# Optimization experiments

Measured on AMD Instinct MI355X. Metric: run time of the kernel, lower is better.

The kernel has to match this reference:

```python
import jax, jax.numpy as jnp
import numpy as np
from functools import partial

VOCAB, D, H, L, T_MAX = 32000, 1024, 16, 8, 1024
HD = D // H
HIDDEN = int(D * 2.67)  # 2734, matches int(n_embd*hidden_mult)


def setup_inputs() -> dict:
    key = jax.random.key(0)
    ks = jax.random.split(key, 9)
    s = 0.02
    return {
        "idx": jax.random.randint(ks[0], (2, 1024), 0, VOCAB),
        "W_emb": jax.random.normal(ks[1], (VOCAB, D), jnp.float32) * s,  # tied with lm_head
        "norm1_w": jnp.ones((L, D), jnp.float32),
        "Wqkv": jax.random.normal(ks[2], (L, D, 3 * D), jnp.float32) * s,
        "Wout": jax.random.normal(ks[3], (L, D, D), jnp.float32) * s,
        "norm2_w": jnp.ones((L, D), jnp.float32),
        "Wg": jax.random.normal(ks[4], (L, D, HIDDEN), jnp.float32) * s,
        "Wu": jax.random.normal(ks[5], (L, D, HIDDEN), jnp.float32) * s,
        "Wd": jax.random.normal(ks[6], (L, HIDDEN, D), jnp.float32) * s,
        "final_norm_w": jnp.ones((D,), jnp.float32),
    }


def _rmsnorm(x, w, eps=1e-6):
    rms = jnp.sqrt(jnp.mean(x * x, axis=-1, keepdims=True) + eps)
    return x / rms * w


def _rope(x, cos_f, sin_f):
    # x: [B,H,T,hd]; cos_f/sin_f: [T, hd//2]
    x1, x2 = x[..., : HD // 2], x[..., HD // 2 :]
    c = cos_f[None, None]
    s = sin_f[None, None]
    return jnp.concatenate([x1 * c - x2 * s, x1 * s + x2 * c], axis=-1)


def _forward(idx, W_emb, norm1_w, Wqkv, Wout, norm2_w, Wg, Wu, Wd, final_norm_w):
    B, T = idx.shape
    # RoPE tables (buffers in the torch module)
    inv_freq = 1.0 / (10000.0 ** (jnp.arange(0, HD, 2, dtype=jnp.float32) / HD))
    ang = jnp.arange(T, dtype=jnp.float32)[:, None] * inv_freq[None, :]  # [T, hd//2]
    cos_f, sin_f = jnp.cos(ang), jnp.sin(ang)
    causal = jnp.tril(jnp.ones((T, T), dtype=bool))  # [T,T]
    scale = 1.0 / jnp.sqrt(jnp.float32(HD))

    def block(x, params):
        n1, wqkv, wout, n2, wg, wu, wd = params
        h = _rmsnorm(x, n1)
        qkv = (h @ wqkv).reshape(B, T, 3, H, HD).transpose(2, 0, 3, 1, 4)  # [3,B,H,T,hd]
        q, k, v = qkv[0], qkv[1], qkv[2]
        q = _rope(q, cos_f, sin_f)
        k = _rope(k, cos_f, sin_f)
        attn = jnp.einsum("bhqd,bhkd->bhqk", q, k) * scale
        attn = jnp.where(causal[None, None], attn, -jnp.inf)
        attn = jax.nn.softmax(attn, axis=-1)
        o = jnp.einsum("bhqk,bhkd->bhqd", attn, v)
        o = o.transpose(0, 2, 1, 3).reshape(B, T, D) @ wout
        x = x + o
        h2 = _rmsnorm(x, n2)
        x = x + (jax.nn.silu(h2 @ wg) * (h2 @ wu)) @ wd
        return x, None

    x = W_emb[idx]  # [B,T,D]
    x, _ = jax.lax.scan(block, x, (norm1_w, Wqkv, Wout, norm2_w, Wg, Wu, Wd))
    x = _rmsnorm(x, final_norm_w)
    return x @ W_emb.T  # tied lm_head -> [B,T,VOCAB]


def reference(idx, W_emb, norm1_w, Wqkv, Wout, norm2_w, Wg, Wu, Wd, final_norm_w):
    return _forward(idx, W_emb, norm1_w, Wqkv, Wout, norm2_w, Wg, Wu, Wd, final_norm_w)
```

## Files before the change

### kernel.cpp

```cpp
#include <hip/hip_runtime.h>
#include <cstdint>
#include <cmath>

#define D_MODEL 1024
#define T_SEQ   1024
#define NHEAD   16
#define NLAYER  8
#define HID     2734
#define HID_PAD 2816
#define NTOK    2048
#define VOCAB   32000

typedef __bf16 bf16x8 __attribute__((ext_vector_type(8)));
typedef __bf16 bf16x4 __attribute__((ext_vector_type(4)));
typedef float  f32x4  __attribute__((ext_vector_type(4)));

__device__ inline bf16x4 to_bf4(float a, float b, float c, float d) {
  bf16x4 t; t[0] = (__bf16)a; t[1] = (__bf16)b; t[2] = (__bf16)c; t[3] = (__bf16)d; return t;
}

__device__ inline void gload16(const __bf16* g, __bf16* l) {
  __builtin_amdgcn_global_load_lds(
      (const __attribute__((address_space(1))) void*)g,
      (__attribute__((address_space(3))) void*)l, 16, 0, 0);
}

__global__ __launch_bounds__(256) void embed_kernel(const int* __restrict__ idx,
                                                    const float* __restrict__ W,
                                                    float* __restrict__ x) {
  int t = blockIdx.x;
  int v = idx[t];
  float4 val = *(const float4*)&W[(size_t)v * D_MODEL + threadIdx.x * 4];
  *(float4*)&x[(size_t)t * D_MODEL + threadIdx.x * 4] = val;
}

__global__ __launch_bounds__(256) void rmsnorm_kernel(const float* __restrict__ x,
                                                      const float* __restrict__ w,
                                                      __bf16* __restrict__ out) {
  int row = blockIdx.x;
  int tid = threadIdx.x;
  float4 v = *(const float4*)&x[(size_t)row * D_MODEL + tid * 4];
  float s = v.x * v.x + v.y * v.y + v.z * v.z + v.w * v.w;
#pragma unroll
  for (int m = 32; m >= 1; m >>= 1) s += __shfl_xor(s, m, 64);
  __shared__ float red[4];
  if ((tid & 63) == 0) red[tid >> 6] = s;
  __syncthreads();
  float tot = red[0] + red[1] + red[2] + red[3];
  float inv = rsqrtf(tot * (1.0f / (float)D_MODEL) + 1e-6f);
  float4 wv = *(const float4*)&w[tid * 4];
  bf16x4 o4 = to_bf4(v.x * inv * wv.x, v.y * inv * wv.y, v.z * inv * wv.z, v.w * inv * wv.w);
  *(bf16x4*)&out[(size_t)row * D_MODEL + tid * 4] = o4;
}

__global__ __launch_bounds__(256) void rope_table_kernel(float* __restrict__ tab) {
  int p = blockIdx.x * 256 + threadIdx.x;
  int t = p >> 5, i = p & 31;
  float freq = exp2f(-(float)i * (13.287712379549449f / 32.0f));
  float sn, cs;
  sincosf((float)t * freq, &sn, &cs);
  tab[p] = cs;
  tab[32768 + p] = sn;
}

__global__ __launch_bounds__(256) void tp5_kernel(
    const float* __restrict__ Wqkv, const float* __restrict__ Wout,
    const float* __restrict__ Wg, const float* __restrict__ Wu,
    const float* __restrict__ Wd,
    __bf16* __restrict__ wqkvT, __bf16* __restrict__ woutT,
    __bf16* __restrict__ wguT, __bf16* __restrict__ wdT) {
  __shared__ __bf16 tile[64][65];
  int t = blockIdx.x;
  const float* in;
  __bf16* out;
  int R, C, Ro, rmul, roff, tr;
  if (t < 768)        { in = Wqkv; out = wqkvT; R = 1024; C = 3072; Ro = 1024; rmul = 1; roff = 0; tr = 16; }
  else if (t < 1024)  { t -= 768;  in = Wout; out = woutT; R = 1024; C = 1024; Ro = 1024; rmul = 1; roff = 0; tr = 16; }
  else if (t < 1728)  { t -= 1024; in = Wg; out = wguT; R = 1024; C = HID; Ro = 1024; rmul = 2; roff = 0; tr = 16; }
  else if (t < 2432)  { t -= 1728; in = Wu; out = wguT; R = 1024; C = HID; Ro = 1024; rmul = 2; roff = 1; tr = 16; }
  else                { t -= 2432; in = Wd; out = wdT; R = HID; C = 1024; Ro = HID_PAD; rmul = 1; roff = 0; tr = 44; }
  int r0 = (t % tr) * 64, c0 = (t / tr) * 64;
  int tid = threadIdx.x;
  bool fullc = (c0 + 64 <= C);
#pragma unroll
  for (int i = 0; i < 4; ++i) {
    int ri = i * 16 + (tid >> 4);
    int ci = (tid & 15) * 4;
    int r = r0 + ri;
    float4 v = {0.f, 0.f, 0.f, 0.f};
    if (r < R) {
      const float* p = in + (size_t)r * C + c0 + ci;
      if (fullc) {
        v = *(const float4*)p;
      } else {
        int c = c0 + ci;
        if (c + 0 < C) v.x = p[0];
        if (c + 1 < C) v.y = p[1];
        if (c + 2 < C) v.z = p[2];
        if (c + 3 < C) v.w = p[3];
      }
    }
    tile[ri][ci + 0] = (__bf16)v.x;
    tile[ri][ci + 1] = (__bf16)v.y;
    tile[ri][ci + 2] = (__bf16)v.z;
    tile[ri][ci + 3] = (__bf16)v.w;
  }
  __syncthreads();
#pragma unroll
  for (int i = 0; i < 4; ++i) {
    int oc = i * 16 + (tid >> 4);
    int orr = (tid & 15) * 4;
    bf16x4 tv;
    tv[0] = tile[orr + 0][oc];
    tv[1] = tile[orr + 1][oc];
    tv[2] = tile[orr + 2][oc];
    tv[3] = tile[orr + 3][oc];
    *(bf16x4*)&out[((size_t)(c0 + oc) * rmul + roff) * Ro + r0 + orr] = tv;
  }
}

__global__ __launch_bounds__(256) void convert_bf16_kernel(const float* __restrict__ in,
                                                           __bf16* __restrict__ out, int n4) {
  for (int i = blockIdx.x * 256 + threadIdx.x; i < n4; i += gridDim.x * 256) {
    float4 v = ((const float4*)in)[i];
    ((bf16x4*)out)[i] = to_bf4(v.x, v.y, v.z, v.w);
  }
}

template <int BM, int BN, int WM, int WN, int EPI>
__global__ __launch_bounds__(WM * WN * 64, 2) void gemm8(
    const __bf16* __restrict__ A, const __bf16* __restrict__ B,
    const float* __restrict__ Cin, void* __restrict__ Cout,
    int K, int ldc) {
  constexpr int NTH = WM * WN * 64;
  constexpr int MF = BM / (16 * WM);
  constexpr int MG = (MF + 3) / 4;
  constexpr int CL = (MF < 4) ? MF : 4;
  constexpr int LA = (BM * 4) / NTH;
  constexpr int LB = (BN * 4) / NTH;
  static_assert(BN / WN == 64, "NF must be 4");
  __shared__ __align__(16) __bf16 lds[(BM + BN) * 128];

  const int tid = threadIdx.x;
  const int lane = tid & 63, wid = tid >> 6;
  const int wr = wid / WN, wn = wid % WN;
  const int lr = lane & 15, lg = lane >> 4;

  const int gx = gridDim.x;
  const int nwg = gx * gridDim.y;
  const int orig = blockIdx.y * gx + blockIdx.x;
  const int q = nwg >> 3, r8 = nwg & 7;
  const int xcd = orig & 7, loc = orig >> 3;
  const int swz = ((xcd < r8) ? xcd * (q + 1) : r8 * (q + 1) + (xcd - r8) * q) + loc;
  const int brow = (swz % gx) * BM;
  const int bcol = (swz / gx) * BN;

  const __bf16* pAg[LA];
  const __bf16* pBg[LB];
  int opA[LA], opB[LB];
#pragma unroll
  for (int i = 0; i < LA; ++i) {
    int p = tid + i * NTH;
    int row = ((p >> 6) << 4) | (p & 15), j = (p >> 4) & 3;
    pAg[i] = A + (size_t)(brow + row) * K + j * 8;
    opA[i] = p * 8;
  }
#pragma unroll
  for (int i = 0; i < LB; ++i) {
    int p = tid + i * NTH;
    int row = ((p >> 6) << 4) | (p & 15), j = (p >> 4) & 3;
    pBg[i] = B + (size_t)(bcol + row) * K + j * 8;
    opB[i] = p * 8;
  }

  const int ntiles = K >> 6;

  auto STAGE_A = [&](int v, int kkq) {
    int vs = v < ntiles ? v : ntiles - 1;
    int ko = vs * 64 + kkq * 32;
    int sa = (v & 1) * (BM * 64) + kkq * (BM * 32);
#pragma unroll
    for (int i = 0; i < LA; ++i) gload16(pAg[i] + ko, lds + sa + opA[i]);
  };
  auto STAGE_B = [&](int v, int kkq) {
    int vs = v < ntiles ? v : ntiles - 1;
    int ko = vs * 64 + kkq * 32;
    int sb = BM * 128 + (v & 1) * (BN * 64) + kkq * (BN * 32);
#pragma unroll
    for (int i = 0; i < LB; ++i) gload16(pBg[i] + ko, lds + sb + opB[i]);
  };

  f32x4 acc[MF][4];
#pragma unroll
  for (int m = 0; m < MF; ++m)
#pragma unroll
    for (int n = 0; n < 4; ++n) acc[m][n] = (f32x4){0.f, 0.f, 0.f, 0.f};

  STAGE_A(0, 0); STAGE_B(0, 0);
  STAGE_A(0, 1); STAGE_B(0, 1);
  STAGE_A(1, 0); STAGE_B(1, 0);

  const int fragoff = lg * 128 + lr * 8;

  if constexpr (MF == 8) {
    for (int u = 0; u < ntiles; ++u) {
      const int buf = u & 1;
#pragma unroll
      for (int kk = 0; kk < 2; ++kk) {
        const int v = (kk == 0) ? u + 1 : u + 2;
        const int kkq = kk ^ 1;
        const __bf16* Ab = lds + buf * (BM * 64) + kk * (BM * 32);
        const __bf16* Bb = lds + BM * 128 + buf * (BN * 64) + kk * (BN * 32);
        asm volatile("s_waitcnt vmcnt(8)" ::: "memory");
        __builtin_amdgcn_sched_barrier(0);
        __builtin_amdgcn_s_barrier();
        __builtin_amdgcn_sched_barrier(0);
        STAGE_A(v, kkq);
        bf16x8 bfr[4], af0[4];
#pragma unroll
        for (int n = 0; n < 4; ++n)
          bfr[n] = *(const bf16x8*)(Bb + (wn * 64 + n * 16) * 32 + fragoff);
#pragma unroll
        for (int i = 0; i < 4; ++i)
          af0[i] = *(const bf16x8*)(Ab + (wr * 128 + i * 16) * 32 + fragoff);
        asm volatile("s_waitcnt lgkmcnt(0)" ::: "memory");
        __builtin_amdgcn_sched_barrier(0);
        __builtin_amdgcn_s_setprio(1);
#pragma unroll
        for (int i = 0; i < 4; ++i)
#pragma unroll
          for (int n = 0; n < 4; ++n)
            acc[i][n] = __builtin_amdgcn_mfma_f32_16x16x32_bf16(af0[i], bfr[n], acc[i][n], 0, 0, 0);
        __builtin_amdgcn_s_setprio(0);
        __builtin_amdgcn_s_barrier();
        STAGE_B(v, kkq);
        bf16x8 af1[4];
#pragma unroll
        for (int i = 0; i < 4; ++i)
          af1[i] = *(const bf16x8*)(Ab + (wr * 128 + 64 + i * 16) * 32 + fragoff);
        asm volatile("s_waitcnt lgkmcnt(0)" ::: "memory");
        __builtin_amdgcn_sched_barrier(0);
        __builtin_amdgcn_s_setprio(1);
#pragma unroll
        for (int i = 0; i < 4; ++i)
#pragma unroll
          for (int n = 0; n < 4; ++n)
            acc[4 + i][n] = __builtin_amdgcn_mfma_f32_16x16x32_bf16(af1[i], bfr[n], acc[4 + i][n], 0, 0, 0);
        __builtin_amdgcn_s_setprio(0);
        __builtin_amdgcn_s_barrier();
      }
    }
  } else {
    for (int u = 0; u < ntiles; ++u) {
      const int buf = u & 1;
#pragma unroll
      for (int kk = 0; kk < 2; ++kk) {
        if constexpr (LA + LB == 3) asm volatile("s_waitcnt vmcnt(6)" ::: "memory");
        else                        asm volatile("s_waitcnt vmcnt(8)" ::: "memory");
        __builtin_amdgcn_sched_barrier(0);
        __builtin_amdgcn_s_barrier();
        __builtin_amdgcn_sched_barrier(0);
        const int v = (kk == 0) ? u + 1 : u + 2;
        const int kkq = kk ^ 1;
        STAGE_A(v, kkq);
        STAGE_B(v, kkq);
        const __bf16* Ab = lds + buf * (BM * 64) + kk * (BM * 32);
        const __bf16* Bb = lds + BM * 128 + buf * (BN * 64) + kk * (BN * 32);
        bf16x8 bfr[4];
#pragma unroll
        for (int n = 0; n < 4; ++n)
          bfr[n] = *(const bf16x8*)(Bb + (wn * 64 + n * 16) * 32 + fragoff);
#pragma unroll
        for (int mg = 0; mg < MG; ++mg) {
          bf16x8 afr[CL];
#pragma unroll
          for (int i = 0; i < CL; ++i)
            afr[i] = *(const bf16x8*)(Ab + (wr * (BM / WM) + (mg * 4 + i) * 16) * 32 + fragoff);
          __builtin_amdgcn_s_setprio(1);
#pragma unroll
          for (int i = 0; i < CL; ++i)
#pragma unroll
            for (int n = 0; n < 4; ++n)
              acc[mg * 4 + i][n] =
                  __builtin_amdgcn_mfma_f32_16x16x32_bf16(afr[i], bfr[n], acc[mg * 4 + i][n], 0, 0, 0);
          __builtin_amdgcn_s_setprio(0);
        }
      }
    }
  }

#pragma unroll
  for (int m = 0; m < MF; ++m) {
#pragma unroll
    for (int n = 0; n < 4; ++n) {
#pragma unroll
      for (int rr = 0; rr < 4; ++rr) {
        int row = brow + wr * (BM / WM) + m * 16 + lg * 4 + rr;
        int col = bcol + wn * 64 + n * 16 + lr;
        size_t off = (size_t)row * ldc + col;
        float vv = acc[m][n][rr];
        if (EPI == 0) {
          ((float*)Cout)[off] = vv;
        } else if (EPI == 1) {
          ((float*)Cout)[off] = Cin[off] + vv;
        } else if (EPI == 2) {
          float gv = Cin[off];
          ((__bf16*)Cout)[off] = (__bf16)(gv / (1.f + __expf(-gv)) * vv);
        } else if (EPI == 3) {
          ((__bf16*)Cout)[off] = (__bf16)vv;
        } else {
          float uv = __shfl_xor(vv, 1);
          if ((lr & 1) == 0) {
            float r = vv / (1.f + __expf(-vv)) * uv;
            ((__bf16*)Cout)[(size_t)row * ldc + (col >> 1)] = (__bf16)r;
          }
        }
      }
    }
  }
}

__device__ inline void rope_chunk(const __bf16* p, const float* __restrict__ tab,
                                  int t, int d0, bf16x8& olo, bf16x8& ohi) {
  bf16x8 a8 = *(const bf16x8*)p;
  bf16x8 b8 = *(const bf16x8*)(p + 32);
  const float* ct = tab + t * 32 + d0;
  const float* st = tab + 32768 + t * 32 + d0;
  float4 c0 = *(const float4*)ct, c1 = *(const float4*)(ct + 4);
  float4 s0 = *(const float4*)st, s1 = *(const float4*)(st + 4);
  float cs[8] = {c0.x, c0.y, c0.z, c0.w, c1.x, c1.y, c1.z, c1.w};
  float ss[8] = {s0.x, s0.y, s0.z, s0.w, s1.x, s1.y, s1.z, s1.w};
#pragma unroll
  for (int j = 0; j < 8; ++j) {
    float av = (float)a8[j], bv = (float)b8[j];
    olo[j] = (__bf16)(av * cs[j] - bv * ss[j]);
    ohi[j] = (__bf16)(av * ss[j] + bv * cs[j]);
  }
}

__global__ __launch_bounds__(256) void prep_kernel(const __bf16* __restrict__ qkv,
                                                   const float* __restrict__ tab,
                                                   __bf16* __restrict__ Qr,
                                                   __bf16* __restrict__ Kr,
                                                   __bf16* __restrict__ Vt) {
  __shared__ __bf16 lsV[64][72];
  const int tid = threadIdx.x;
  const int bh = blockIdx.y, b = bh >> 4, h = bh & 15;
  const int t0 = blockIdx.x * 64;
  const size_t qbase = (size_t)b * T_SEQ * 3072 + h * 64;

  int row = tid >> 2, pc = tid & 3;
  int t = t0 + row;
  int tl = t & 1023;
  {
    int d0 = pc * 8;
    bf16x8 olo, ohi;
    rope_chunk(qkv + qbase + (size_t)t * 3072 + d0, tab, tl, d0, olo, ohi);
    __bf16* qo = Qr + ((size_t)bh * T_SEQ + t) * 64;
    *(bf16x8*)(qo + d0) = olo;
    *(bf16x8*)(qo + d0 + 32) = ohi;
    rope_chunk(qkv + qbase + (size_t)t * 3072 + 1024 + d0, tab, tl, d0, olo, ohi);
    __bf16* ko = Kr + ((size_t)bh * T_SEQ + t) * 64;
    *(bf16x8*)(ko + d0) = olo;
    *(bf16x8*)(ko + d0 + 32) = ohi;
  }
  {
    int c = pc * 16;
    bf16x8 v0 = *(const bf16x8*)(qkv + qbase + (size_t)t * 3072 + 2048 + c);
    bf16x8 v1 = *(const bf16x8*)(qkv + qbase + (size_t)t * 3072 + 2048 + c + 8);
    *(bf16x8*)&lsV[row][c] = v0;
    *(bf16x8*)&lsV[row][c + 8] = v1;
  }
  __syncthreads();
  {
    int d = tid >> 2, tc = (tid & 3) * 16;
    bf16x8 o0, o1;
#pragma unroll
    for (int j = 0; j < 8; ++j) o0[j] = lsV[tc + j][d];
#pragma unroll
    for (int j = 0; j < 8; ++j) o1[j] = lsV[tc + 8 + j][d];
    __bf16* vo = Vt + ((size_t)bh * 64 + d) * T_SEQ + t0 + tc;
    *(bf16x8*)vo = o0;
    *(bf16x8*)(vo + 8) = o1;
  }
}

__global__ __launch_bounds__(256) void attn_kernel(const __bf16* __restrict__ Qr,
                                                   const __bf16* __restrict__ Kr,
                                                   const __bf16* __restrict__ Vt,
                                                   __bf16* __restrict__ o) {
  __shared__ __align__(16) __bf16 lds[28672];
  const int tid = threadIdx.x;
  const int lane = tid & 63, w = tid >> 6;
  const int lr = lane & 15, lg = lane >> 4;
  const int bh = blockIdx.y, b = bh >> 4, h = bh & 15;
  const int qb = blockIdx.x, q0 = qb * 64;
  const __bf16* Qg = Qr + ((size_t)bh * T_SEQ + q0) * 64;
  const __bf16* Kg = Kr + (size_t)bh * T_SEQ * 64;
  const __bf16* Vg = Vt + (size_t)bh * 64 * T_SEQ;
  const float scale = 0.125f;

  {
    int row = ((tid >> 6) << 4) | (tid & 15);
    int j = (tid >> 4) & 3;
    gload16(Qg + row * 64 + j * 8, lds + tid * 8);
    gload16(Qg + row * 64 + 32 + j * 8, lds + 2048 + tid * 8);
  }

  f32x4 accO[4];
#pragma unroll
  for (int n = 0; n < 4; ++n) accO[n] = (f32x4){0.f, 0.f, 0.f, 0.f};
  float mrow[4], lrow[4];
#pragma unroll
  for (int r = 0; r < 4; ++r) { mrow[r] = -1e30f; lrow[r] = 0.f; }

  const int ntile = ((q0 + 63) >> 7) + 1;
  __bf16* Pw = lds + 20480 + w * 2048;

  for (int tt = 0; tt < ntile; ++tt) {
    const int j0 = tt * 128;
    __syncthreads();
#pragma unroll
    for (int i = 0; i < 2; ++i) {
      int p = tid + i * 256;
      int row = ((p >> 6) << 4) | (p & 15), j = (p >> 4) & 3;
      const __bf16* src = Kg + (size_t)(j0 + row) * 64 + j * 8;
      gload16(src, lds + 4096 + p * 8);
      gload16(src + 32, lds + 8192 + p * 8);
    }
#pragma unroll
    for (int s = 0; s < 4; ++s) {
      int d = ((tid >> 6) << 4) | (tid & 15), j = (tid >> 4) & 3;
      gload16(Vg + (size_t)d * T_SEQ + j0 + s * 32 + j * 8, lds + 12288 + s * 2048 + tid * 8);
    }
    __syncthreads();

    f32x4 s4[8];
#pragma unroll
    for (int n = 0; n < 8; ++n) s4[n] = (f32x4){0.f, 0.f, 0.f, 0.f};
#pragma unroll
    for (int kk = 0; kk < 2; ++kk) {
      bf16x8 aq = *(const bf16x8*)(lds + kk * 2048 + (w * 64 + lg * 16 + lr) * 8);
      __builtin_amdgcn_s_setprio(1);
#pragma unroll
      for (int jf = 0; jf < 8; ++jf) {
        bf16x8 bk = *(const bf16x8*)(lds + 4096 + kk * 4096 + (jf * 64 + lg * 16 + lr) * 8);
        s4[jf] = __builtin_amdgcn_mfma_f32_16x16x32_bf16(aq, bk, s4[jf], 0, 0, 0);
      }
      __builtin_amdgcn_s_setprio(0);
    }

    float pm[4];
#pragma unroll
    for (int r = 0; r < 4; ++r) pm[r] = -1e30f;
#pragma unroll
    for (int jf = 0; jf < 8; ++jf) {
      int gj = j0 + jf * 16 + lr;
#pragma unroll
      for (int r = 0; r < 4; ++r) {
        int gq = q0 + w * 16 + lg * 4 + r;
        float sv = s4[jf][r] * scale;
        if (gj > gq) sv = -1e30f;
        s4[jf][r] = sv;
        pm[r] = fmaxf(pm[r], sv);
      }
    }
#pragma unroll
    for (int r = 0; r < 4; ++r) {
#pragma unroll
      for (int m = 8; m >= 1; m >>= 1) pm[r] = fmaxf(pm[r], __shfl_xor(pm[r], m, 64));
    }
    float alpha[4];
#pragma unroll
    for (int r = 0; r < 4; ++r) {
      float mn = fmaxf(mrow[r], pm[r]);
      alpha[r] = expf(mrow[r] - mn);
      mrow[r] = mn;
    }
    float ps[4] = {0.f, 0.f, 0.f, 0.f};
#pragma unroll
    for (int jf = 0; jf < 8; ++jf) {
#pragma unroll
      for (int r = 0; r < 4; ++r) {
        float p = expf(s4[jf][r] - mrow[r]);
        s4[jf][r] = p;
        ps[r] += p;
      }
    }
#pragma unroll
    for (int r = 0; r < 4; ++r) {
#pragma unroll
      for (int m = 8; m >= 1; m >>= 1) ps[r] += __shfl_xor(ps[r], m, 64);
      lrow[r] = lrow[r] * alpha[r] + ps[r];
    }
#pragma unroll
    for (int n = 0; n < 4; ++n) {
#pragma unroll
      for (int r = 0; r < 4; ++r) accO[n][r] *= alpha[r];
    }

#pragma unroll
    for (int jf = 0; jf < 8; ++jf) {
      int s = jf >> 1;
      int rem = ((jf & 1) << 4) + lr;
      int base = s * 512 + (rem >> 3) * 128 + (rem & 7);
#pragma unroll
      for (int r = 0; r < 4; ++r) {
        int qloc = lg * 4 + r;
        Pw[base + qloc * 8] = (__bf16)s4[jf][r];
      }
    }
    asm volatile("s_waitcnt lgkmcnt(0)" ::: "memory");
    __builtin_amdgcn_sched_barrier(0);

#pragma unroll
    for (int s = 0; s < 4; ++s) {
      bf16x8 pa = *(const bf16x8*)(Pw + s * 512 + (lg * 16 + lr) * 8);
      __builtin_amdgcn_s_setprio(1);
#pragma unroll
      for (int nd = 0; nd < 4; ++nd) {
        bf16x8 bv = *(const bf16x8*)(lds + 12288 + s * 2048 + (nd * 64 + lg * 16 + lr) * 8);
        accO[nd] = __builtin_amdgcn_mfma_f32_16x16x32_bf16(pa, bv, accO[nd], 0, 0, 0);
      }
      __builtin_amdgcn_s_setprio(0);
    }
  }

#pragma unroll
  for (int nd = 0; nd < 4; ++nd) {
#pragma unroll
    for (int r = 0; r < 4; ++r) {
      int gq = q0 + w * 16 + lg * 4 + r;
      float val = accO[nd][r] / lrow[r];
      o[(size_t)(b * T_SEQ + gq) * D_MODEL + h * 64 + nd * 16 + lr] = (__bf16)val;
    }
  }
}

extern "C" void kernel_launch(void* const* d_in, const int* in_sizes, int n_in,
                              void* d_out, int out_size, void* d_ws, size_t ws_size,
                              hipStream_t stream) {
  const int*   idx     = (const int*)d_in[0];
  const float* W_emb   = (const float*)d_in[1];
  const float* norm1_w = (const float*)d_in[2];
  const float* Wqkv    = (const float*)d_in[3];
  const float* Wout    = (const float*)d_in[4];
  const float* norm2_w = (const float*)d_in[5];
  const float* Wg      = (const float*)d_in[6];
  const float* Wu      = (const float*)d_in[7];
  const float* Wd      = (const float*)d_in[8];
  const float* fnorm   = (const float*)d_in[9];
  float* out = (float*)d_out;

  float*  x    = (float*)d_ws;
  float*  tab  = x + (size_t)NTOK * D_MODEL;
  __bf16* qkvb = (__bf16*)(tab + 2 * 32768);
  __bf16* hb   = qkvb + (size_t)NTOK * 3 * D_MODEL;
  __bf16* ob   = hb + (size_t)NTOK * D_MODEL;
  __bf16* ga   = ob + (size_t)NTOK * D_MODEL;
  __bf16* Qrb  = ga + (size_t)NTOK * HID_PAD;
  __bf16* Krb  = Qrb + (size_t)32 * T_SEQ * 64;
  __bf16* Vtb  = Krb + (size_t)32 * T_SEQ * 64;
  __bf16* wbuf = Vtb + (size_t)32 * T_SEQ * 64;

  __bf16* wqkvT = wbuf;
  __bf16* woutT = wqkvT + (size_t)3 * D_MODEL * D_MODEL;
  __bf16* wguT  = woutT + (size_t)D_MODEL * D_MODEL;
  __bf16* wdT   = wguT + (size_t)2 * HID_PAD * D_MODEL;

  embed_kernel<<<NTOK, 256, 0, stream>>>(idx, W_emb, x);
  rope_table_kernel<<<128, 256, 0, stream>>>(tab);

  for (int l = 0; l < NLAYER; ++l) {
    tp5_kernel<<<3136, 256, 0, stream>>>(
        Wqkv + (size_t)l * D_MODEL * 3 * D_MODEL,
        Wout + (size_t)l * D_MODEL * D_MODEL,
        Wg + (size_t)l * D_MODEL * HID,
        Wu + (size_t)l * D_MODEL * HID,
        Wd + (size_t)l * HID * D_MODEL,
        wqkvT, woutT, wguT, wdT);

    rmsnorm_kernel<<<NTOK, 256, 0, stream>>>(x, norm1_w + (size_t)l * D_MODEL, hb);
    gemm8<128, 256, 2, 4, 3><<<dim3(16, 12), 512, 0, stream>>>(
        hb, wqkvT, nullptr, qkvb, D_MODEL, 3 * D_MODEL);
    prep_kernel<<<dim3(16, 32), 256, 0, stream>>>(qkvb, tab, Qrb, Krb, Vtb);
    attn_kernel<<<dim3(16, 32), 256, 0, stream>>>(Qrb, Krb, Vtb, ob);
    gemm8<128, 64, 4, 1, 1><<<dim3(16, 16), 256, 0, stream>>>(
        ob, woutT, x, x, D_MODEL, D_MODEL);
    rmsnorm_kernel<<<NTOK, 256, 0, stream>>>(x, norm2_w + (size_t)l * D_MODEL, hb);
    gemm8<256, 256, 2, 4, 4><<<dim3(8, 22), 512, 0, stream>>>(
        hb, wguT, nullptr, ga, D_MODEL, HID_PAD);
    gemm8<128, 64, 4, 1, 1><<<dim3(16, 16), 256, 0, stream>>>(
        ga, wdT, x, x, HID_PAD, D_MODEL);
  }

  rmsnorm_kernel<<<NTOK, 256, 0, stream>>>(x, fnorm, hb);
  convert_bf16_kernel<<<2048, 256, 0, stream>>>(W_emb, wbuf, VOCAB * D_MODEL / 4);
  gemm8<256, 256, 2, 4, 0><<<dim3(8, 125), 512, 0, stream>>>(
      hb, wbuf, nullptr, out, D_MODEL, VOCAB);
}
```

Before: 1.780 ms.

## Fuse RoPE and V transpose into QKV GEMM epilogue; pair causal attention blocks

The QKV GEMM gets a new epilogue that applies rotary embedding to Q and K and writes the transposed V directly into the attention layouts. This removes the separate prep kernel and the intermediate bf16 QKV buffer. Separately, the attention kernel now processes two complementary query blocks per workgroup (qp and 15-qp) to balance causal work, which halves the grid. The trade-offs are narrower, less coalesced epilogue stores and fewer attention workgroups.

```diff
diff --git a/kernel.cpp b/kernel.cpp
--- a/kernel.cpp
+++ b/kernel.cpp
@@ -131,7 +131,9 @@
 __global__ __launch_bounds__(WM * WN * 64, 2) void gemm8(
     const __bf16* __restrict__ A, const __bf16* __restrict__ B,
     const float* __restrict__ Cin, void* __restrict__ Cout,
-    int K, int ldc) {
+    int K, int ldc,
+    const float* __restrict__ Tab, __bf16* __restrict__ Qr,
+    __bf16* __restrict__ Kr, __bf16* __restrict__ Vt) {
   constexpr int NTH = WM * WN * 64;
   constexpr int MF = BM / (16 * WM);
   constexpr int MG = (MF + 3) / 4;
@@ -289,99 +291,66 @@
     }
   }
 
-#pragma unroll
-  for (int m = 0; m < MF; ++m) {
-#pragma unroll
-    for (int n = 0; n < 4; ++n) {
-#pragma unroll
-      for (int rr = 0; rr < 4; ++rr) {
-        int row = brow + wr * (BM / WM) + m * 16 + lg * 4 + rr;
-        int col = bcol + wn * 64 + n * 16 + lr;
-        size_t off = (size_t)row * ldc + col;
-        float vv = acc[m][n][rr];
-        if (EPI == 0) {
-          ((float*)Cout)[off] = vv;
-        } else if (EPI == 1) {
-          ((float*)Cout)[off] = Cin[off] + vv;
-        } else if (EPI == 2) {
-          float gv = Cin[off];
-          ((__bf16*)Cout)[off] = (__bf16)(gv / (1.f + __expf(-gv)) * vv);
-        } else if (EPI == 3) {
-          ((__bf16*)Cout)[off] = (__bf16)vv;
-        } else {
-          float uv = __shfl_xor(vv, 1);
-          if ((lr & 1) == 0) {
-            float r = vv / (1.f + __expf(-vv)) * uv;
-            ((__bf16*)Cout)[(size_t)row * ldc + (col >> 1)] = (__bf16)r;
+  if constexpr (EPI == 5) {
+    const int colw = bcol + wn * 64;
+    const int secw = colw >> 10;
+    const int h = (colw >> 6) & 15;
+#pragma unroll
+    for (int m = 0; m < MF; ++m) {
+      int row0 = brow + wr * (BM / WM) + m * 16 + lg * 4;
+      int bb = row0 >> 10;
+      int t0 = row0 & 1023;
+      int bh = bb * 16 + h;
+      if (secw < 2) {
+        __bf16* base = (secw == 0 ? Qr : Kr) + ((size_t)bh * T_SEQ + t0) * 64;
+#pragma unroll
+        for (int n = 0; n < 2; ++n) {
+          int din = n * 16 + lr;
+#pragma unroll
+          for (int rr = 0; rr < 4; ++rr) {
+            float a = acc[m][n][rr], b2 = acc[m][n + 2][rr];
+            float cs = Tab[(t0 + rr) * 32 + din];
+            float sn = Tab[32768 + (t0 + rr) * 32 + din];
+            base[(size_t)rr * 64 + din]      = (__bf16)(a * cs - b2 * sn);
+            base[(size_t)rr * 64 + din + 32] = (__bf16)(a * sn + b2 * cs);
           }
         }
-      }
-    }
-  }
-}
-
-__device__ inline void rope_chunk(const __bf16* p, const float* __restrict__ tab,
-                                  int t, int d0, bf16x8& olo, bf16x8& ohi) {
-  bf16x8 a8 = *(const bf16x8*)p;
-  bf16x8 b8 = *(const bf16x8*)(p + 32);
-  const float* ct = tab + t * 32 + d0;
-  const float* st = tab + 32768 + t * 32 + d0;
-  float4 c0 = *(const float4*)ct, c1 = *(const float4*)(ct + 4);
-  float4 s0 = *(const float4*)st, s1 = *(const float4*)(st + 4);
-  float cs[8] = {c0.x, c0.y, c0.z, c0.w, c1.x, c1.y, c1.z, c1.w};
-  float ss[8] = {s0.x, s0.y, s0.z, s0.w, s1.x, s1.y, s1.z, s1.w};
-#pragma unroll
-  for (int j = 0; j < 8; ++j) {
-    float av = (float)a8[j], bv = (float)b8[j];
-    olo[j] = (__bf16)(av * cs[j] - bv * ss[j]);
-    ohi[j] = (__bf16)(av * ss[j] + bv * cs[j]);
-  }
-}
-
-__global__ __launch_bounds__(256) void prep_kernel(const __bf16* __restrict__ qkv,
-                                                   const float* __restrict__ tab,
-                                                   __bf16* __restrict__ Qr,
-                                                   __bf16* __restrict__ Kr,
-                                                   __bf16* __restrict__ Vt) {
-  __shared__ __bf16 lsV[64][72];
-  const int tid = threadIdx.x;
-  const int bh = blockIdx.y, b = bh >> 4, h = bh & 15;
-  const int t0 = blockIdx.x * 64;
-  const size_t qbase = (size_t)b * T_SEQ * 3072 + h * 64;
-
-  int row = tid >> 2, pc = tid & 3;
-  int t = t0 + row;
-  int tl = t & 1023;
-  {
-    int d0 = pc * 8;
-    bf16x8 olo, ohi;
-    rope_chunk(qkv + qbase + (size_t)t * 3072 + d0, tab, tl, d0, olo, ohi);
-    __bf16* qo = Qr + ((size_t)bh * T_SEQ + t) * 64;
-    *(bf16x8*)(qo + d0) = olo;
-    *(bf16x8*)(qo + d0 + 32) = ohi;
-    rope_chunk(qkv + qbase + (size_t)t * 3072 + 1024 + d0, tab, tl, d0, olo, ohi);
-    __bf16* ko = Kr + ((size_t)bh * T_SEQ + t) * 64;
-    *(bf16x8*)(ko + d0) = olo;
-    *(bf16x8*)(ko + d0 + 32) = ohi;
-  }
-  {
-    int c = pc * 16;
-    bf16x8 v0 = *(const bf16x8*)(qkv + qbase + (size_t)t * 3072 + 2048 + c);
-    bf16x8 v1 = *(const bf16x8*)(qkv + qbase + (size_t)t * 3072 + 2048 + c + 8);
-    *(bf16x8*)&lsV[row][c] = v0;
-    *(bf16x8*)&lsV[row][c + 8] = v1;
-  }
-  __syncthreads();
-  {
-    int d = tid >> 2, tc = (tid & 3) * 16;
-    bf16x8 o0, o1;
-#pragma unroll
-    for (int j = 0; j < 8; ++j) o0[j] = lsV[tc + j][d];
-#pragma unroll
-    for (int j = 0; j < 8; ++j) o1[j] = lsV[tc + 8 + j][d];
-    __bf16* vo = Vt + ((size_t)bh * 64 + d) * T_SEQ + t0 + tc;
-    *(bf16x8*)vo = o0;
-    *(bf16x8*)(vo + 8) = o1;
+      } else {
+#pragma unroll
+        for (int n = 0; n < 4; ++n) {
+          int din = n * 16 + lr;
+          bf16x4 pk;
+#pragma unroll
+          for (int rr = 0; rr < 4; ++rr) pk[rr] = (__bf16)acc[m][n][rr];
+          *(bf16x4*)&Vt[((size_t)bh * 64 + din) * T_SEQ + t0] = pk;
+        }
+      }
+    }
+  } else {
+#pragma unroll
+    for (int m = 0; m < MF; ++m) {
+#pragma unroll
+      for (int n = 0; n < 4; ++n) {
+#pragma unroll
+        for (int rr = 0; rr < 4; ++rr) {
+          int row = brow + wr * (BM / WM) + m * 16 + lg * 4 + rr;
+          int col = bcol + wn * 64 + n * 16 + lr;
+          size_t off = (size_t)row * ldc + col;
+          float vv = acc[m][n][rr];
+          if (EPI == 0) {
+            ((float*)Cout)[off] = vv;
+          } else if (EPI == 1) {
+            ((float*)Cout)[off] = Cin[off] + vv;
+          } else {
+            float uv = __shfl_xor(vv, 1);
+            if ((lr & 1) == 0) {
+              float r = vv / (1.f + __expf(-vv)) * uv;
+              ((__bf16*)Cout)[(size_t)row * ldc + (col >> 1)] = (__bf16)r;
+            }
+          }
+        }
+      }
+    }
   }
 }
 
@@ -394,145 +363,151 @@
   const int lane = tid & 63, w = tid >> 6;
   const int lr = lane & 15, lg = lane >> 4;
   const int bh = blockIdx.y, b = bh >> 4, h = bh & 15;
-  const int qb = blockIdx.x, q0 = qb * 64;
-  const __bf16* Qg = Qr + ((size_t)bh * T_SEQ + q0) * 64;
+  const int qp = blockIdx.x;
   const __bf16* Kg = Kr + (size_t)bh * T_SEQ * 64;
   const __bf16* Vg = Vt + (size_t)bh * 64 * T_SEQ;
   const float scale = 0.125f;
-
-  {
-    int row = ((tid >> 6) << 4) | (tid & 15);
-    int j = (tid >> 4) & 3;
-    gload16(Qg + row * 64 + j * 8, lds + tid * 8);
-    gload16(Qg + row * 64 + 32 + j * 8, lds + 2048 + tid * 8);
-  }
-
-  f32x4 accO[4];
-#pragma unroll
-  for (int n = 0; n < 4; ++n) accO[n] = (f32x4){0.f, 0.f, 0.f, 0.f};
-  float mrow[4], lrow[4];
-#pragma unroll
-  for (int r = 0; r < 4; ++r) { mrow[r] = -1e30f; lrow[r] = 0.f; }
-
-  const int ntile = ((q0 + 63) >> 7) + 1;
   __bf16* Pw = lds + 20480 + w * 2048;
 
-  for (int tt = 0; tt < ntile; ++tt) {
-    const int j0 = tt * 128;
+  for (int qs = 0; qs < 2; ++qs) {
+    const int qb = qs ? (15 - qp) : qp;
+    const int q0 = qb * 64;
+    const __bf16* Qg = Qr + ((size_t)bh * T_SEQ + q0) * 64;
+
     __syncthreads();
-#pragma unroll
-    for (int i = 0; i < 2; ++i) {
-      int p = tid + i * 256;
-      int row = ((p >> 6) << 4) | (p & 15), j = (p >> 4) & 3;
-      const __bf16* src = Kg + (size_t)(j0 + row) * 64 + j * 8;
-      gload16(src, lds + 4096 + p * 8);
-      gload16(src + 32, lds + 8192 + p * 8);
-    }
-#pragma unroll
-    for (int s = 0; s < 4; ++s) {
-      int d = ((tid >> 6) << 4) | (tid & 15), j = (tid >> 4) & 3;
-      gload16(Vg + (size_t)d * T_SEQ + j0 + s * 32 + j * 8, lds + 12288 + s * 2048 + tid * 8);
-    }
-    __syncthreads();
-
-    f32x4 s4[8];
-#pragma unroll
-    for (int n = 0; n < 8; ++n) s4[n] = (f32x4){0.f, 0.f, 0.f, 0.f};
-#pragma unroll
-    for (int kk = 0; kk < 2; ++kk) {
-      bf16x8 aq = *(const bf16x8*)(lds + kk * 2048 + (w * 64 + lg * 16 + lr) * 8);
-      __builtin_amdgcn_s_setprio(1);
+    {
+      int row = ((tid >> 6) << 4) | (tid & 15);
+      int j = (tid >> 4) & 3;
+      gload16(Qg + row * 64 + j * 8, lds + tid * 8);
+      gload16(Qg + row * 64 + 32 + j * 8, lds + 2048 + tid * 8);
+    }
+
+    f32x4 accO[4];
+#pragma unroll
+    for (int n = 0; n < 4; ++n) accO[n] = (f32x4){0.f, 0.f, 0.f, 0.f};
+    float mrow[4], lrow[4];
+#pragma unroll
+    for (int r = 0; r < 4; ++r) { mrow[r] = -1e30f; lrow[r] = 0.f; }
+
+    const int ntile = ((q0 + 63) >> 7) + 1;
+
+    for (int tt = 0; tt < ntile; ++tt) {
+      const int j0 = tt * 128;
+      __syncthreads();
+#pragma unroll
+      for (int i = 0; i < 2; ++i) {
+        int p = tid + i * 256;
+        int row = ((p >> 6) << 4) | (p & 15), j = (p >> 4) & 3;
+        const __bf16* src = Kg + (size_t)(j0 + row) * 64 + j * 8;
+        gload16(src, lds + 4096 + p * 8);
+        gload16(src + 32, lds + 8192 + p * 8);
+      }
+#pragma unroll
+      for (int s = 0; s < 4; ++s) {
+        int d = ((tid >> 6) << 4) | (tid & 15), j = (tid >> 4) & 3;
+        gload16(Vg + (size_t)d * T_SEQ + j0 + s * 32 + j * 8, lds + 12288 + s * 2048 + tid * 8);
+      }
+      __syncthreads();
+
+      f32x4 s4[8];
+#pragma unroll
+      for (int n = 0; n < 8; ++n) s4[n] = (f32x4){0.f, 0.f, 0.f, 0.f};
+#pragma unroll
+      for (int kk = 0; kk < 2; ++kk) {
+        bf16x8 aq = *(const bf16x8*)(lds + kk * 2048 + (w * 64 + lg * 16 + lr) * 8);
+        __builtin_amdgcn_s_setprio(1);
+#pragma unroll
+        for (int jf = 0; jf < 8; ++jf) {
+          bf16x8 bk = *(const bf16x8*)(lds + 4096 + kk * 4096 + (jf * 64 + lg * 16 + lr) * 8);
+          s4[jf] = __builtin_amdgcn_mfma_f32_16x16x32_bf16(aq, bk, s4[jf], 0, 0, 0);
+        }
+        __builtin_amdgcn_s_setprio(0);
+      }
+
+      float pm[4];
+#pragma unroll
+      for (int r = 0; r < 4; ++r) pm[r] = -1e30f;
 #pragma unroll
       for (int jf = 0; jf < 8; ++jf) {
-        bf16x8 bk = *(const bf16x8*)(lds + 4096 + kk * 4096 + (jf * 64 + lg * 16 + lr) * 8);
-        s4[jf] = __builtin_amdgcn_mfma_f32_16x16x32_bf16(aq, bk, s4[jf], 0, 0, 0);
-      }
-      __builtin_amdgcn_s_setprio(0);
-    }
-
-    float pm[4];
-#pragma unroll
-    for (int r = 0; r < 4; ++r) pm[r] = -1e30f;
-#pragma unroll
-    for (int jf = 0; jf < 8; ++jf) {
-      int gj = j0 + jf * 16 + lr;
+        int gj = j0 + jf * 16 + lr;
+#pragma unroll
+        for (int r = 0; r < 4; ++r) {
+          int gq = q0 + w * 16 + lg * 4 + r;
+          float sv = s4[jf][r] * scale;
+          if (gj > gq) sv = -1e30f;
+          s4[jf][r] = sv;
+          pm[r] = fmaxf(pm[r], sv);
+        }
+      }
+#pragma unroll
+      for (int r = 0; r < 4; ++r) {
+#pragma unroll
+        for (int m = 8; m >= 1; m >>= 1) pm[r] = fmaxf(pm[r], __shfl_xor(pm[r], m, 64));
+      }
+      float alpha[4];
+#pragma unroll
+      for (int r = 0; r < 4; ++r) {
+        float mn = fmaxf(mrow[r], pm[r]);
+        alpha[r] = expf(mrow[r] - mn);
+        mrow[r] = mn;
+      }
+      float ps[4] = {0.f, 0.f, 0.f, 0.f};
+#pragma unroll
+      for (int jf = 0; jf < 8; ++jf) {
+#pragma unroll
+        for (int r = 0; r < 4; ++r) {
+          float p = expf(s4[jf][r] - mrow[r]);
+          s4[jf][r] = p;
+          ps[r] += p;
+        }
+      }
+#pragma unroll
+      for (int r = 0; r < 4; ++r) {
+#pragma unroll
+        for (int m = 8; m >= 1; m >>= 1) ps[r] += __shfl_xor(ps[r], m, 64);
+        lrow[r] = lrow[r] * alpha[r] + ps[r];
+      }
+#pragma unroll
+      for (int n = 0; n < 4; ++n) {
+#pragma unroll
+        for (int r = 0; r < 4; ++r) accO[n][r] *= alpha[r];
+      }
+
+#pragma unroll
+      for (int jf = 0; jf < 8; ++jf) {
+        int s = jf >> 1;
+        int rem = ((jf & 1) << 4) + lr;
+        int base = s * 512 + (rem >> 3) * 128 + (rem & 7);
+#pragma unroll
+        for (int r = 0; r < 4; ++r) {
+          int qloc = lg * 4 + r;
+          Pw[base + qloc * 8] = (__bf16)s4[jf][r];
+        }
+      }
+      asm volatile("s_waitcnt lgkmcnt(0)" ::: "memory");
+      __builtin_amdgcn_sched_barrier(0);
+
+#pragma unroll
+      for (int s = 0; s < 4; ++s) {
+        bf16x8 pa = *(const bf16x8*)(Pw + s * 512 + (lg * 16 + lr) * 8);
+        __builtin_amdgcn_s_setprio(1);
+#pragma unroll
+        for (int nd = 0; nd < 4; ++nd) {
+          bf16x8 bv = *(const bf16x8*)(lds + 12288 + s * 2048 + (nd * 64 + lg * 16 + lr) * 8);
+          accO[nd] = __builtin_amdgcn_mfma_f32_16x16x32_bf16(pa, bv, accO[nd], 0, 0, 0);
+        }
+        __builtin_amdgcn_s_setprio(0);
+      }
+    }
+
+#pragma unroll
+    for (int nd = 0; nd < 4; ++nd) {
 #pragma unroll
       for (int r = 0; r < 4; ++r) {
         int gq = q0 + w * 16 + lg * 4 + r;
-        float sv = s4[jf][r] * scale;
-        if (gj > gq) sv = -1e30f;
-        s4[jf][r] = sv;
-        pm[r] = fmaxf(pm[r], sv);
-      }
-    }
-#pragma unroll
-    for (int r = 0; r < 4; ++r) {
-#pragma unroll
-      for (int m = 8; m >= 1; m >>= 1) pm[r] = fmaxf(pm[r], __shfl_xor(pm[r], m, 64));
-    }
-    float alpha[4];
-#pragma unroll
-    for (int r = 0; r < 4; ++r) {
-      float mn = fmaxf(mrow[r], pm[r]);
-      alpha[r] = expf(mrow[r] - mn);
-      mrow[r] = mn;
-    }
-    float ps[4] = {0.f, 0.f, 0.f, 0.f};
-#pragma unroll
-    for (int jf = 0; jf < 8; ++jf) {
-#pragma unroll
-      for (int r = 0; r < 4; ++r) {
-        float p = expf(s4[jf][r] - mrow[r]);
-        s4[jf][r] = p;
-        ps[r] += p;
-      }
-    }
-#pragma unroll
-    for (int r = 0; r < 4; ++r) {
-#pragma unroll
-      for (int m = 8; m >= 1; m >>= 1) ps[r] += __shfl_xor(ps[r], m, 64);
-      lrow[r] = lrow[r] * alpha[r] + ps[r];
-    }
-#pragma unroll
-    for (int n = 0; n < 4; ++n) {
-#pragma unroll
-      for (int r = 0; r < 4; ++r) accO[n][r] *= alpha[r];
-    }
-
-#pragma unroll
-    for (int jf = 0; jf < 8; ++jf) {
-      int s = jf >> 1;
-      int rem = ((jf & 1) << 4) + lr;
-      int base = s * 512 + (rem >> 3) * 128 + (rem & 7);
-#pragma unroll
-      for (int r = 0; r < 4; ++r) {
-        int qloc = lg * 4 + r;
-        Pw[base + qloc * 8] = (__bf16)s4[jf][r];
-      }
-    }
-    asm volatile("s_waitcnt lgkmcnt(0)" ::: "memory");
-    __builtin_amdgcn_sched_barrier(0);
-
-#pragma unroll
-    for (int s = 0; s < 4; ++s) {
-      bf16x8 pa = *(const bf16x8*)(Pw + s * 512 + (lg * 16 + lr) * 8);
-      __builtin_amdgcn_s_setprio(1);
-#pragma unroll
-      for (int nd = 0; nd < 4; ++nd) {
-        bf16x8 bv = *(const bf16x8*)(lds + 12288 + s * 2048 + (nd * 64 + lg * 16 + lr) * 8);
-        accO[nd] = __builtin_amdgcn_mfma_f32_16x16x32_bf16(pa, bv, accO[nd], 0, 0, 0);
-      }
-      __builtin_amdgcn_s_setprio(0);
-    }
-  }
-
-#pragma unroll
-  for (int nd = 0; nd < 4; ++nd) {
-#pragma unroll
-    for (int r = 0; r < 4; ++r) {
-      int gq = q0 + w * 16 + lg * 4 + r;
-      float val = accO[nd][r] / lrow[r];
-      o[(size_t)(b * T_SEQ + gq) * D_MODEL + h * 64 + nd * 16 + lr] = (__bf16)val;
+        float val = accO[nd][r] / lrow[r];
+        o[(size_t)(b * T_SEQ + gq) * D_MODEL + h * 64 + nd * 16 + lr] = (__bf16)val;
+      }
     }
   }
 }
@@ -554,8 +529,7 @@
 
   float*  x    = (float*)d_ws;
   float*  tab  = x + (size_t)NTOK * D_MODEL;
-  __bf16* qkvb = (__bf16*)(tab + 2 * 32768);
-  __bf16* hb   = qkvb + (size_t)NTOK * 3 * D_MODEL;
+  __bf16* hb   = (__bf16*)(tab + 2 * 32768);
   __bf16* ob   = hb + (size_t)NTOK * D_MODEL;
   __bf16* ga   = ob + (size_t)NTOK * D_MODEL;
   __bf16* Qrb  = ga + (size_t)NTOK * HID_PAD;
@@ -581,21 +555,20 @@
         wqkvT, woutT, wguT, wdT);
 
     rmsnorm_kernel<<<NTOK, 256, 0, stream>>>(x, norm1_w + (size_t)l * D_MODEL, hb);
-    gemm8<128, 256, 2, 4, 3><<<dim3(16, 12), 512, 0, stream>>>(
-        hb, wqkvT, nullptr, qkvb, D_MODEL, 3 * D_MODEL);
-    prep_kernel<<<dim3(16, 32), 256, 0, stream>>>(qkvb, tab, Qrb, Krb, Vtb);
-    attn_kernel<<<dim3(16, 32), 256, 0, stream>>>(Qrb, Krb, Vtb, ob);
+    gemm8<128, 256, 2, 4, 5><<<dim3(16, 12), 512, 0, stream>>>(
+        hb, wqkvT, nullptr, nullptr, D_MODEL, 3 * D_MODEL, tab, Qrb, Krb, Vtb);
+    attn_kernel<<<dim3(8, 32), 256, 0, stream>>>(Qrb, Krb, Vtb, ob);
     gemm8<128, 64, 4, 1, 1><<<dim3(16, 16), 256, 0, stream>>>(
-        ob, woutT, x, x, D_MODEL, D_MODEL);
+        ob, woutT, x, x, D_MODEL, D_MODEL, nullptr, nullptr, nullptr, nullptr);
     rmsnorm_kernel<<<NTOK, 256, 0, stream>>>(x, norm2_w + (size_t)l * D_MODEL, hb);
     gemm8<256, 256, 2, 4, 4><<<dim3(8, 22), 512, 0, stream>>>(
-        hb, wguT, nullptr, ga, D_MODEL, HID_PAD);
+        hb, wguT, nullptr, ga, D_MODEL, HID_PAD, nullptr, nullptr, nullptr, nullptr);
     gemm8<128, 64, 4, 1, 1><<<dim3(16, 16), 256, 0, stream>>>(
-        ga, wdT, x, x, HID_PAD, D_MODEL);
+        ga, wdT, x, x, HID_PAD, D_MODEL, nullptr, nullptr, nullptr, nullptr);
   }
 
   rmsnorm_kernel<<<NTOK, 256, 0, stream>>>(x, fnorm, hb);
   convert_bf16_kernel<<<2048, 256, 0, stream>>>(W_emb, wbuf, VOCAB * D_MODEL / 4);
   gemm8<256, 256, 2, 4, 0><<<dim3(8, 125), 512, 0, stream>>>(
-      hb, wbuf, nullptr, out, D_MODEL, VOCAB);
-}
+      hb, wbuf, nullptr, out, D_MODEL, VOCAB, nullptr, nullptr, nullptr, nullptr);
+}
```

Result: faster. 1.734 ms (-2.6%).
